# Kernel optimization log

Measured on AMD Instinct MI355X. Metric: run time of the kernel, lower is better.

Reference implementation:

```python
import jax, jax.numpy as jnp
import numpy as np

B, T, PHYS = 256, 64, 3        # batch of initial conditions, time steps, physical dim
LAT, NN, NHID = 8, 128, 3      # latent dim, hidden width, num hidden layers
WIN, PRED = 32, 64             # Hankel window, num_pred_steps


def _mlp(x, w_in, b_in, w_h, b_h, w_out, b_out):
    # Dense stack: relu hidden layers, linear output (ae_output_activation='linear')
    h = jax.nn.relu(x @ w_in + b_in)
    for i in range(w_h.shape[0]):
        h = jax.nn.relu(h @ w_h[i] + b_h[i])
    return h @ w_out + b_out


def _hankel_dmd(y):
    # y: [B, L, T] latent trajectories (already transposed as in call())
    Bsz, L, Tn = y.shape
    R = Tn - (WIN - 1)                                   # num_rows_hankel
    # Vectorized Hankel build (replaces nested TensorArray loops):
    idx = jnp.arange(R)[:, None] + jnp.arange(WIN)[None, :]
    H = y[:, :, idx].reshape(Bsz, L * R, WIN)
    Ym, Yp = H[:, :, :-1], H[:, :, 1:]
    # Exact DMD operator A = Yp V Sig^-1 U^H (full M x M, as in the TF code)
    U, sig, Vh = jnp.linalg.svd(Ym, full_matrices=False)
    V = jnp.swapaxes(Vh, -1, -2)
    A = Yp @ (V / sig[:, None, :]) @ jnp.swapaxes(U, -1, -2)     # [B, M, M]
    A = jax.lax.stop_gradient(A)   # no-op in fwd; eig has no JAX grad rule
    evals, evecs = jnp.linalg.eig(A)                             # complex64: [B,M], [B,M,M]
    Phi = jnp.linalg.solve(evecs, Ym.astype(evecs.dtype))
    y0 = Phi[:, :, 0]                                            # [B, M]
    evecs_s = evecs[:, ::R, :]                                   # stride = R -> [B, L, M]
    # Vectorized replacement of the sequential recon loop: evals^k for k=0..P-1
    powers = evals[:, None, :] ** jnp.arange(PRED)[None, :, None]  # [B, P, M]
    modes = powers * y0[:, None, :]                                # [B, P, M]
    recon = jnp.real(jnp.einsum('blm,bpm->bpl', evecs_s, modes))   # [B, P, L]
    return recon


def setup_inputs() -> dict:
    ks = jax.random.split(jax.random.key(0), 8)

    def w(k, fi, fo):
        return jax.random.normal(k, (fi, fo), jnp.float32) / np.sqrt(fi)

    def wh(k, f):
        return jax.random.normal(k, (NHID, f, f), jnp.float32) / np.sqrt(f)

    return {
        'x': jax.random.normal(ks[0], (B, T, PHYS), jnp.float32),
        'enc_w_in': w(ks[1], PHYS, NN), 'enc_b_in': jnp.zeros((NN,), jnp.float32),
        'enc_w_h': wh(ks[2], NN), 'enc_b_h': jnp.zeros((NHID, NN), jnp.float32),
        'enc_w_out': w(ks[3], NN, LAT), 'enc_b_out': jnp.zeros((LAT,), jnp.float32),
        'dec_w_in': w(ks[4], LAT, NN), 'dec_b_in': jnp.zeros((NN,), jnp.float32),
        'dec_w_h': wh(ks[5], NN), 'dec_b_h': jnp.zeros((NHID, NN), jnp.float32),
        'dec_w_out': w(ks[6], NN, PHYS), 'dec_b_out': jnp.zeros((PHYS,), jnp.float32),
    }


def reference(x, enc_w_in, enc_b_in, enc_w_h, enc_b_h, enc_w_out, enc_b_out,
              dec_w_in, dec_b_in, dec_w_h, dec_b_h, dec_w_out, dec_b_out):
    y = _mlp(x, enc_w_in, enc_b_in, enc_w_h, enc_b_h, enc_w_out, enc_b_out)        # [B, T, LAT]
    x_ae = _mlp(y, dec_w_in, dec_b_in, dec_w_h, dec_b_h, dec_w_out, dec_b_out)     # [B, T, PHYS]
    y_adv = _hankel_dmd(jnp.swapaxes(y, 1, 2))                                     # [B, PRED, LAT]
    x_adv = _mlp(y_adv, dec_w_in, dec_b_in, dec_w_h, dec_b_h, dec_w_out, dec_b_out)  # [B, PRED, PHYS]
    return (y, x_ae, x_adv, y_adv)
```

## Files before the change

kernel.cpp:

```cpp
#include <hip/hip_runtime.h>
#include <math.h>

namespace {
constexpr int kB = 256;
constexpr int kT = 64;
constexpr int kPhys = 3;
constexpr int kLat = 8;
constexpr int kNN = 128;
constexpr int kWin = 32;
constexpr int kPred = 64;
constexpr int kHRow = 132;
constexpr int kThreads = 1024;
constexpr int kWUnit = 8 * 4 * 64 * 8;
constexpr int kUS = 50688;
}

typedef short bf16x8 __attribute__((ext_vector_type(8)));
typedef float f32x4 __attribute__((ext_vector_type(4)));

__device__ __forceinline__ double rdlane_f64(double x, int l) {
  const long long v = __double_as_longlong(x);
  const int lo = __builtin_amdgcn_readlane((int)(unsigned int)(v & 0xffffffffll), l);
  const int hi = __builtin_amdgcn_readlane((int)(v >> 32), l);
  const long long r = (((long long)hi) << 32) | (unsigned long long)(unsigned int)lo;
  return __longlong_as_double(r);
}

__device__ __forceinline__ unsigned rneb(float f) {
  const unsigned u = __float_as_uint(f);
  return (u + 0x7fffu + ((u >> 16) & 1u)) >> 16;
}
__device__ __forceinline__ void split3(float a, short& s1, short& s2, short& s3) {
  const unsigned b1 = rneb(a);
  const float f1 = __uint_as_float(b1 << 16);
  const float r1 = a - f1;
  const unsigned b2 = rneb(r1);
  const float f2 = __uint_as_float(b2 << 16);
  s1 = (short)b1; s2 = (short)b2; s3 = (short)rneb(r1 - f2);
}
__device__ __forceinline__ void split2(float a, short& s1, short& s2) {
  const unsigned b1 = rneb(a);
  const float f1 = __uint_as_float(b1 << 16);
  s1 = (short)b1; s2 = (short)rneb(a - f1);
}

__global__ __launch_bounds__(256) void split_weights_kernel(
    const float* __restrict__ ewh, const float* __restrict__ dwh,
    short* __restrict__ wfrag)
{
  const int gid = blockIdx.x * 256 + threadIdx.x;
  const int l = gid & 63;
  const int q = (gid >> 6) & 3;
  const int n = (gid >> 8) & 7;
  const int layer = gid >> 11;
  const bool enc = layer < 3;
  const float* __restrict__ W = enc ? (ewh + (size_t)layer * kNN * kNN)
                                    : (dwh + (size_t)(layer - 3) * kNN * kNN);
  const int colg = 16 * n + (l & 15);
  const int krow = 8 * (l >> 4);
  bf16x8 p1, p2, p3;
#pragma unroll
  for (int e = 0; e < 8; ++e) {
    const float wv = W[(32 * q + krow + e) * kNN + colg];
    short s1, s2, s3; split3(wv, s1, s2, s3);
    p1[e] = s1; p2[e] = s2; p3[e] = s3;
  }
  const int off = ((n * 4 + q) * 64 + l) * 8;
  if (enc) {
    const size_t base = (size_t)(layer * 3) * kWUnit;
    *(bf16x8*)&wfrag[base + off] = p1;
    *(bf16x8*)&wfrag[base + kWUnit + off] = p2;
    *(bf16x8*)&wfrag[base + 2 * kWUnit + off] = p3;
  } else {
    const size_t base = (size_t)(9 + (layer - 3) * 2) * kWUnit;
    *(bf16x8*)&wfrag[base + off] = p1;
    *(bf16x8*)&wfrag[base + kWUnit + off] = p2;
  }
}

template<int MPW, int SPLITS, bool TO_FRAG>
__device__ __forceinline__ void mfma_scatter(
    const short* __restrict__ Bfrag, const float* __restrict__ bias,
    const short* __restrict__ fragIn, void* __restrict__ out, int tid)
{
  constexpr int MT = 2 * MPW;
  constexpr int PLANE = MT * 4 * 64 * 8;
  const int w = tid >> 6, l = tid & 63;
  const int n = w & 7, m0 = (w >> 3) * MPW;
  const int colg = 16 * n + (l & 15);
  bf16x8 B1[4], B2[4], B3[4];
#pragma unroll
  for (int q = 0; q < 4; ++q) {
    const int boff = ((n * 4 + q) * 64 + l) * 8;
    B1[q] = *(const bf16x8*)&Bfrag[boff];
    B2[q] = *(const bf16x8*)&Bfrag[kWUnit + boff];
    if constexpr (SPLITS == 3) B3[q] = *(const bf16x8*)&Bfrag[2 * kWUnit + boff];
  }
  const float bj = bias[colg];
  f32x4 acc[MPW];
#pragma unroll
  for (int mi = 0; mi < MPW; ++mi) acc[mi] = {bj, bj, bj, bj};
#pragma unroll
  for (int q = 0; q < 4; ++q) {
#pragma unroll
    for (int mi = 0; mi < MPW; ++mi) {
      const int o = (((m0 + mi) * 4 + q) * 64 + l) * 8;
      const bf16x8 a1 = *(const bf16x8*)&fragIn[o];
      const bf16x8 a2 = *(const bf16x8*)&fragIn[PLANE + o];
      acc[mi] = __builtin_amdgcn_mfma_f32_16x16x32_bf16(a1, B1[q], acc[mi], 0, 0, 0);
      acc[mi] = __builtin_amdgcn_mfma_f32_16x16x32_bf16(a1, B2[q], acc[mi], 0, 0, 0);
      acc[mi] = __builtin_amdgcn_mfma_f32_16x16x32_bf16(a2, B1[q], acc[mi], 0, 0, 0);
      if constexpr (SPLITS == 3) {
        const bf16x8 a3 = *(const bf16x8*)&fragIn[2 * PLANE + o];
        acc[mi] = __builtin_amdgcn_mfma_f32_16x16x32_bf16(a1, B3[q], acc[mi], 0, 0, 0);
        acc[mi] = __builtin_amdgcn_mfma_f32_16x16x32_bf16(a2, B2[q], acc[mi], 0, 0, 0);
        acc[mi] = __builtin_amdgcn_mfma_f32_16x16x32_bf16(a3, B1[q], acc[mi], 0, 0, 0);
      }
    }
  }
  const int rbase = (l >> 4) * 4;
  if constexpr (TO_FRAG) {
    short* __restrict__ f = (short*)out;
    const int qt = colg >> 5, sub = (colg >> 3) & 3, et = colg & 7;
#pragma unroll
    for (int mi = 0; mi < MPW; ++mi)
#pragma unroll
      for (int r = 0; r < 4; ++r) {
        const float v = fmaxf(acc[mi][r], 0.f);
        const int off = (((m0 + mi) * 4 + qt) * 64 + (rbase + r + 16 * sub)) * 8 + et;
        if constexpr (SPLITS == 3) {
          short s1, s2, s3; split3(v, s1, s2, s3);
          f[off] = s1; f[PLANE + off] = s2; f[2 * PLANE + off] = s3;
        } else {
          short s1, s2; split2(v, s1, s2);
          f[off] = s1; f[PLANE + off] = s2;
        }
      }
  } else {
    float* __restrict__ hb = (float*)out;
#pragma unroll
    for (int mi = 0; mi < MPW; ++mi)
#pragma unroll
      for (int r = 0; r < 4; ++r)
        hb[(16 * (m0 + mi) + rbase + r) * kHRow + colg] = fmaxf(acc[mi][r], 0.f);
  }
}

__global__ __launch_bounds__(kThreads, 4) void fused_kernel(
    const float* __restrict__ x,
    const float* __restrict__ ewin, const float* __restrict__ ebin,
    const float* __restrict__ ebh,
    const float* __restrict__ ewout,const float* __restrict__ ebout,
    const float* __restrict__ dwin, const float* __restrict__ dbin,
    const float* __restrict__ dbh,
    const float* __restrict__ dwout,const float* __restrict__ dbout,
    const short* __restrict__ wfrag,
    float* __restrict__ y_g, float* __restrict__ xae_g,
    float* __restrict__ xadv_g, float* __restrict__ yadv_g)
{
  __shared__ __align__(16) char US1[kUS];
  __shared__ __align__(16) char US2[kUS];
  __shared__ float ybuf[kT * kLat];
  __shared__ float yadv2[kWin * kLat];

  const int tid = threadIdx.x;
  const int b = blockIdx.x;

  double* dmd  = (double*)US1;
  double* yd   = dmd;
  double* P    = dmd + 520;
  double* Corr = dmd + 2664;
  double* KTm  = dmd + 3720;
  double* Dv   = dmd + 4743;

  constexpr int PE = 4 * 4 * 64 * 8;
  constexpr int PD = 6 * 4 * 64 * 8;

  {
    short* __restrict__ f = (short*)US1;
    const float* __restrict__ xg = x + (size_t)b * kT * kPhys;
    const int j = tid & 127, rg = tid >> 7;
    const float w0 = ewin[j], w1 = ewin[kNN + j], w2 = ewin[2 * kNN + j];
    const float bj = ebin[j];
    const int qt = j >> 5, sub = (j >> 3) & 3, et = j & 7;
#pragma unroll
    for (int rr = 0; rr < 8; ++rr) {
      const int r = rg * 8 + rr;
      const float* __restrict__ xr = xg + r * 3;
      const float a = fmaxf(bj + xr[0] * w0 + xr[1] * w1 + xr[2] * w2, 0.f);
      short s1, s2, s3; split3(a, s1, s2, s3);
      const int off = (((r >> 4) * 4 + qt) * 64 + ((r & 15) + 16 * sub)) * 8 + et;
      f[off] = s1; f[PE + off] = s2; f[2 * PE + off] = s3;
    }
  }
  __syncthreads();

  mfma_scatter<2, 3, true >(wfrag + (size_t)0 * kWUnit, ebh + 0 * kNN, (short*)US1, US2, tid);
  __syncthreads();
  mfma_scatter<2, 3, true >(wfrag + (size_t)3 * kWUnit, ebh + 1 * kNN, (short*)US2, US1, tid);
  __syncthreads();
  mfma_scatter<2, 3, false>(wfrag + (size_t)6 * kWUnit, ebh + 2 * kNN, (short*)US1, US2, tid);
  __syncthreads();

  if (tid < 512) {
    const float* __restrict__ hb = (const float*)US2;
    const int r = tid >> 3, o = tid & 7;
    float a = ebout[o];
    for (int k4 = 0; k4 < kNN; k4 += 4) {
      const float4 hv = *(const float4*)&hb[r * kHRow + k4];
      a += hv.x * ewout[(k4 + 0) * kLat + o] + hv.y * ewout[(k4 + 1) * kLat + o]
         + hv.z * ewout[(k4 + 2) * kLat + o] + hv.w * ewout[(k4 + 3) * kLat + o];
    }
    ybuf[r * kLat + o] = a;
    y_g[(size_t)b * kT * kLat + tid] = a;
    yd[o * 65 + r] = (double)a;
  }
  __syncthreads();

  {
    for (int idx = tid; idx < 32 * 64; idx += kThreads) {
      const int d = idx >> 6, t = idx & 63;
      if (t + d < kT) {
        double s = 0.0;
#pragma unroll
        for (int l = 0; l < kLat; ++l) s += yd[l * 65 + t] * yd[l * 65 + t + d];
        P[d * 67 + t] = s;
      }
    }
    __syncthreads();

    {
      const int a = tid >> 5, c = tid & 31;
      const int d = (c >= a) ? (c - a) : (a - c);
      const int base = (c >= a) ? a : c;
      double s0 = 0.0, s1 = 0.0;
#pragma unroll
      for (int r = 0; r < 32; r += 2) { s0 += P[d * 67 + base + r]; s1 += P[d * 67 + base + r + 1]; }
      Corr[a * 33 + c] = s0 + s1 + P[d * 67 + base + 32];
    }
    __syncthreads();

    if (tid < 64) {
      const int lane = tid;
      const int colidx = (lane <= 30) ? lane : (lane <= 61 ? lane - 30 : 1);
      double m[31];
#pragma unroll
      for (int i = 0; i < 31; ++i) m[i] = Corr[i * 33 + colidx];
#pragma unroll
      for (int k = 0; k < 31; ++k) {
        const double piv = rdlane_f64(m[k], k);
        const double pinv = 1.0 / piv;
        m[k] *= pinv;
#pragma unroll
        for (int i = 0; i < 31; ++i) {
          if (i == k) continue;
          const double bci = rdlane_f64(m[i], k);
          m[i] = fma(-bci, m[k], m[i]);
        }
      }
      if (lane >= 31 && lane < 62) {
        const int c = lane - 31;
#pragma unroll
        for (int i = 0; i < 31; ++i) KTm[i * 33 + c] = m[i];
      }
      const int ri = (lane < 31) ? lane : 0;
      double Kr[31];
#pragma unroll
      for (int j = 0; j < 31; ++j) Kr[j] = KTm[ri * 33 + j];

      double dv = Kr[30];
      if (lane < 31) Dv[0 * 33 + lane] = dv;
      for (int k = 0; k < 31; ++k) {
        double a0 = 0.0, a1 = 0.0, a2 = 0.0, a3 = 0.0;
#pragma unroll
        for (int j = 0; j < 31; ++j) {
          const double dj = rdlane_f64(dv, j);
          if ((j & 3) == 0) a0 = fma(Kr[j], dj, a0);
          else if ((j & 3) == 1) a1 = fma(Kr[j], dj, a1);
          else if ((j & 3) == 2) a2 = fma(Kr[j], dj, a2);
          else a3 = fma(Kr[j], dj, a3);
        }
        dv = (a0 + a1) + (a2 + a3);
        if (lane < 31) Dv[(k + 1) * 33 + lane] = dv;
      }
    }
    __syncthreads();

    float* __restrict__ ob = yadv_g + (size_t)b * kPred * kLat;
    if (tid < 256) {
      ob[tid] = ybuf[tid];
    } else if (tid < 512) {
      const int q = tid - 256;
      const int k = q >> 3, l = q & 7;
      double a0 = 0.0, a1 = 0.0, a2 = 0.0, a3 = 0.0;
#pragma unroll
      for (int j = 0; j < 31; ++j) {
        const double t = yd[l * 65 + j + 1];
        if ((j & 3) == 0) a0 = fma(t, Dv[k * 33 + j], a0);
        else if ((j & 3) == 1) a1 = fma(t, Dv[k * 33 + j], a1);
        else if ((j & 3) == 2) a2 = fma(t, Dv[k * 33 + j], a2);
        else a3 = fma(t, Dv[k * 33 + j], a3);
      }
      const float v = (float)((a0 + a1) + (a2 + a3));
      ob[256 + q] = v;
      yadv2[q] = v;
    }
    __syncthreads();
  }

  {
    short* __restrict__ f = (short*)US2;
    const int j = tid & 127, rg = tid >> 7;
    float wr[kLat];
#pragma unroll
    for (int k = 0; k < kLat; ++k) wr[k] = dwin[k * kNN + j];
    const float bj = dbin[j];
    const int qt = j >> 5, sub = (j >> 3) & 3, et = j & 7;
#pragma unroll
    for (int rr = 0; rr < 12; ++rr) {
      const int r = rg * 12 + rr;
      const float* __restrict__ src = (r < kT) ? &ybuf[r * kLat] : &yadv2[(r - kT) * kLat];
      float a = bj;
#pragma unroll
      for (int k = 0; k < kLat; ++k) a += src[k] * wr[k];
      a = fmaxf(a, 0.f);
      short s1, s2; split2(a, s1, s2);
      const int off = (((r >> 4) * 4 + qt) * 64 + ((r & 15) + 16 * sub)) * 8 + et;
      f[off] = s1; f[PD + off] = s2;
    }
  }
  __syncthreads();

  mfma_scatter<3, 2, true >(wfrag + (size_t)9  * kWUnit, dbh + 0 * kNN, (short*)US2, US1, tid);
  __syncthreads();
  mfma_scatter<3, 2, true >(wfrag + (size_t)11 * kWUnit, dbh + 1 * kNN, (short*)US1, US2, tid);
  __syncthreads();
  mfma_scatter<3, 2, false>(wfrag + (size_t)13 * kWUnit, dbh + 2 * kNN, (short*)US2, US1, tid);
  __syncthreads();

  if (tid < 96 * kPhys) {
    const float* __restrict__ hb = (const float*)US1;
    const int r = tid / 3, o = tid - r * 3;
    float a = dbout[o];
    for (int k4 = 0; k4 < kNN; k4 += 4) {
      const float4 hv = *(const float4*)&hb[r * kHRow + k4];
      a += hv.x * dwout[(k4 + 0) * kPhys + o] + hv.y * dwout[(k4 + 1) * kPhys + o]
         + hv.z * dwout[(k4 + 2) * kPhys + o] + hv.w * dwout[(k4 + 3) * kPhys + o];
    }
    if (r < kT) {
      xae_g[(size_t)b * kT * kPhys + tid] = a;
      if (r < kWin) xadv_g[(size_t)b * kT * kPhys + tid] = a;
    } else {
      const int rr = r - kT + kWin;
      xadv_g[(size_t)b * kT * kPhys + rr * kPhys + o] = a;
    }
  }
}

extern "C" void kernel_launch(void* const* d_in, const int* in_sizes, int n_in,
                              void* d_out, int out_size, void* d_ws, size_t ws_size,
                              hipStream_t stream)
{
  const float* x         = (const float*)d_in[0];
  const float* enc_w_in  = (const float*)d_in[1];
  const float* enc_b_in  = (const float*)d_in[2];
  const float* enc_w_h   = (const float*)d_in[3];
  const float* enc_b_h   = (const float*)d_in[4];
  const float* enc_w_out = (const float*)d_in[5];
  const float* enc_b_out = (const float*)d_in[6];
  const float* dec_w_in  = (const float*)d_in[7];
  const float* dec_b_in  = (const float*)d_in[8];
  const float* dec_w_h   = (const float*)d_in[9];
  const float* dec_b_h   = (const float*)d_in[10];
  const float* dec_w_out = (const float*)d_in[11];
  const float* dec_b_out = (const float*)d_in[12];

  float* out   = (float*)d_out;
  float* y     = out;
  float* x_ae  = out + (size_t)kB * kT * kLat;
  float* x_adv = x_ae + (size_t)kB * kT * kPhys;
  float* y_adv = x_adv + (size_t)kB * kT * kPhys;

  short* wfrag = (short*)d_ws;

  split_weights_kernel<<<48, 256, 0, stream>>>(enc_w_h, dec_w_h, wfrag);
  fused_kernel<<<kB, kThreads, 0, stream>>>(
      x, enc_w_in, enc_b_in, enc_b_h, enc_w_out, enc_b_out,
      dec_w_in, dec_b_in, dec_b_h, dec_w_out, dec_b_out,
      wfrag, y, x_ae, x_adv, y_adv);
}
```

Measured before the change: 55.89 us.

## Split fused kernel into encoder, DMD, and decoder kernels with row-split blocks

```diff
diff --git a/kernel.cpp b/kernel.cpp
--- a/kernel.cpp
+++ b/kernel.cpp
@@ -10,9 +10,7 @@
 constexpr int kWin = 32;
 constexpr int kPred = 64;
 constexpr int kHRow = 132;
-constexpr int kThreads = 1024;
 constexpr int kWUnit = 8 * 4 * 64 * 8;
-constexpr int kUS = 50688;
 }
 
 typedef short bf16x8 __attribute__((ext_vector_type(8)));
@@ -78,15 +76,13 @@
   }
 }
 
-template<int MPW, int SPLITS, bool TO_FRAG>
-__device__ __forceinline__ void mfma_scatter(
+template<int MT, int SPLITS, bool TO_FRAG>
+__device__ __forceinline__ void mfma_layer8(
     const short* __restrict__ Bfrag, const float* __restrict__ bias,
     const short* __restrict__ fragIn, void* __restrict__ out, int tid)
 {
-  constexpr int MT = 2 * MPW;
   constexpr int PLANE = MT * 4 * 64 * 8;
-  const int w = tid >> 6, l = tid & 63;
-  const int n = w & 7, m0 = (w >> 3) * MPW;
+  const int n = (tid >> 6) & 7, l = tid & 63;
   const int colg = 16 * n + (l & 15);
   bf16x8 B1[4], B2[4], B3[4];
 #pragma unroll
@@ -97,14 +93,14 @@
     if constexpr (SPLITS == 3) B3[q] = *(const bf16x8*)&Bfrag[2 * kWUnit + boff];
   }
   const float bj = bias[colg];
-  f32x4 acc[MPW];
-#pragma unroll
-  for (int mi = 0; mi < MPW; ++mi) acc[mi] = {bj, bj, bj, bj};
+  f32x4 acc[MT];
+#pragma unroll
+  for (int mi = 0; mi < MT; ++mi) acc[mi] = {bj, bj, bj, bj};
 #pragma unroll
   for (int q = 0; q < 4; ++q) {
 #pragma unroll
-    for (int mi = 0; mi < MPW; ++mi) {
-      const int o = (((m0 + mi) * 4 + q) * 64 + l) * 8;
+    for (int mi = 0; mi < MT; ++mi) {
+      const int o = ((mi * 4 + q) * 64 + l) * 8;
       const bf16x8 a1 = *(const bf16x8*)&fragIn[o];
       const bf16x8 a2 = *(const bf16x8*)&fragIn[PLANE + o];
       acc[mi] = __builtin_amdgcn_mfma_f32_16x16x32_bf16(a1, B1[q], acc[mi], 0, 0, 0);
@@ -123,11 +119,11 @@
     short* __restrict__ f = (short*)out;
     const int qt = colg >> 5, sub = (colg >> 3) & 3, et = colg & 7;
 #pragma unroll
-    for (int mi = 0; mi < MPW; ++mi)
+    for (int mi = 0; mi < MT; ++mi)
 #pragma unroll
       for (int r = 0; r < 4; ++r) {
         const float v = fmaxf(acc[mi][r], 0.f);
-        const int off = (((m0 + mi) * 4 + qt) * 64 + (rbase + r + 16 * sub)) * 8 + et;
+        const int off = ((mi * 4 + qt) * 64 + (rbase + r + 16 * sub)) * 8 + et;
         if constexpr (SPLITS == 3) {
           short s1, s2, s3; split3(v, s1, s2, s3);
           f[off] = s1; f[PLANE + off] = s2; f[2 * PLANE + off] = s3;
@@ -139,46 +135,29 @@
   } else {
     float* __restrict__ hb = (float*)out;
 #pragma unroll
-    for (int mi = 0; mi < MPW; ++mi)
+    for (int mi = 0; mi < MT; ++mi)
 #pragma unroll
       for (int r = 0; r < 4; ++r)
-        hb[(16 * (m0 + mi) + rbase + r) * kHRow + colg] = fmaxf(acc[mi][r], 0.f);
-  }
-}
-
-__global__ __launch_bounds__(kThreads, 4) void fused_kernel(
+        hb[(16 * mi + rbase + r) * kHRow + colg] = fmaxf(acc[mi][r], 0.f);
+  }
+}
+
+__global__ __launch_bounds__(512, 4) void enc_kernel(
     const float* __restrict__ x,
     const float* __restrict__ ewin, const float* __restrict__ ebin,
     const float* __restrict__ ebh,
     const float* __restrict__ ewout,const float* __restrict__ ebout,
-    const float* __restrict__ dwin, const float* __restrict__ dbin,
-    const float* __restrict__ dbh,
-    const float* __restrict__ dwout,const float* __restrict__ dbout,
-    const short* __restrict__ wfrag,
-    float* __restrict__ y_g, float* __restrict__ xae_g,
-    float* __restrict__ xadv_g, float* __restrict__ yadv_g)
-{
-  __shared__ __align__(16) char US1[kUS];
-  __shared__ __align__(16) char US2[kUS];
-  __shared__ float ybuf[kT * kLat];
-  __shared__ float yadv2[kWin * kLat];
-
+    const short* __restrict__ wfrag, float* __restrict__ y_g)
+{
+  constexpr int PE = 2 * 4 * 64 * 8;
+  __shared__ __align__(16) char US1[24576];
+  __shared__ __align__(16) char US2[24576];
   const int tid = threadIdx.x;
-  const int b = blockIdx.x;
-
-  double* dmd  = (double*)US1;
-  double* yd   = dmd;
-  double* P    = dmd + 520;
-  double* Corr = dmd + 2664;
-  double* KTm  = dmd + 3720;
-  double* Dv   = dmd + 4743;
-
-  constexpr int PE = 4 * 4 * 64 * 8;
-  constexpr int PD = 6 * 4 * 64 * 8;
+  const int b = blockIdx.x >> 1;
+  const int r0 = (blockIdx.x & 1) * 32;
 
   {
     short* __restrict__ f = (short*)US1;
-    const float* __restrict__ xg = x + (size_t)b * kT * kPhys;
     const int j = tid & 127, rg = tid >> 7;
     const float w0 = ewin[j], w1 = ewin[kNN + j], w2 = ewin[2 * kNN + j];
     const float bj = ebin[j];
@@ -186,7 +165,7 @@
 #pragma unroll
     for (int rr = 0; rr < 8; ++rr) {
       const int r = rg * 8 + rr;
-      const float* __restrict__ xr = xg + r * 3;
+      const float* __restrict__ xr = x + ((size_t)b * kT + r0 + r) * kPhys;
       const float a = fmaxf(bj + xr[0] * w0 + xr[1] * w1 + xr[2] * w2, 0.f);
       short s1, s2, s3; split3(a, s1, s2, s3);
       const int off = (((r >> 4) * 4 + qt) * 64 + ((r & 15) + 16 * sub)) * 8 + et;
@@ -194,15 +173,14 @@
     }
   }
   __syncthreads();
-
-  mfma_scatter<2, 3, true >(wfrag + (size_t)0 * kWUnit, ebh + 0 * kNN, (short*)US1, US2, tid);
-  __syncthreads();
-  mfma_scatter<2, 3, true >(wfrag + (size_t)3 * kWUnit, ebh + 1 * kNN, (short*)US2, US1, tid);
-  __syncthreads();
-  mfma_scatter<2, 3, false>(wfrag + (size_t)6 * kWUnit, ebh + 2 * kNN, (short*)US1, US2, tid);
-  __syncthreads();
-
-  if (tid < 512) {
+  mfma_layer8<2, 3, true >(wfrag + (size_t)0 * kWUnit, ebh + 0 * kNN, (short*)US1, US2, tid);
+  __syncthreads();
+  mfma_layer8<2, 3, true >(wfrag + (size_t)3 * kWUnit, ebh + 1 * kNN, (short*)US2, US1, tid);
+  __syncthreads();
+  mfma_layer8<2, 3, false>(wfrag + (size_t)6 * kWUnit, ebh + 2 * kNN, (short*)US1, US2, tid);
+  __syncthreads();
+
+  if (tid < 256) {
     const float* __restrict__ hb = (const float*)US2;
     const int r = tid >> 3, o = tid & 7;
     float a = ebout[o];
@@ -211,105 +189,143 @@
       a += hv.x * ewout[(k4 + 0) * kLat + o] + hv.y * ewout[(k4 + 1) * kLat + o]
          + hv.z * ewout[(k4 + 2) * kLat + o] + hv.w * ewout[(k4 + 3) * kLat + o];
     }
-    ybuf[r * kLat + o] = a;
-    y_g[(size_t)b * kT * kLat + tid] = a;
-    yd[o * 65 + r] = (double)a;
-  }
-  __syncthreads();
+    y_g[(size_t)b * kT * kLat + (r0 + r) * kLat + o] = a;
+  }
+}
+
+__global__ __launch_bounds__(512) void dmd_kernel(const float* __restrict__ y_g,
+                                                  float* __restrict__ yadv_g)
+{
+  __shared__ __align__(16) char US[46400];
+  double* dmd  = (double*)US;
+  double* yd   = dmd;
+  double* P    = dmd + 520;
+  double* Corr = dmd + 2664;
+  double* KTm  = dmd + 3720;
+  double* Dv   = dmd + 4743;
+  const int tid = threadIdx.x;
+  const int b = blockIdx.x;
+  const float* __restrict__ yb = y_g + (size_t)b * kT * kLat;
 
   {
-    for (int idx = tid; idx < 32 * 64; idx += kThreads) {
-      const int d = idx >> 6, t = idx & 63;
-      if (t + d < kT) {
-        double s = 0.0;
-#pragma unroll
-        for (int l = 0; l < kLat; ++l) s += yd[l * 65 + t] * yd[l * 65 + t + d];
-        P[d * 67 + t] = s;
+    const int r = tid >> 3, o = tid & 7;
+    yd[o * 65 + r] = (double)yb[tid];
+  }
+  __syncthreads();
+
+  for (int idx = tid; idx < 32 * 64; idx += 512) {
+    const int d = idx >> 6, t = idx & 63;
+    if (t + d < kT) {
+      double s = 0.0;
+#pragma unroll
+      for (int l = 0; l < kLat; ++l) s += yd[l * 65 + t] * yd[l * 65 + t + d];
+      P[d * 67 + t] = s;
+    }
+  }
+  __syncthreads();
+
+  for (int idx = tid; idx < 32 * 32; idx += 512) {
+    const int a = idx >> 5, c = idx & 31;
+    const int d = (c >= a) ? (c - a) : (a - c);
+    const int base = (c >= a) ? a : c;
+    double s0 = 0.0, s1 = 0.0;
+#pragma unroll
+    for (int r = 0; r < 32; r += 2) { s0 += P[d * 67 + base + r]; s1 += P[d * 67 + base + r + 1]; }
+    Corr[a * 33 + c] = s0 + s1 + P[d * 67 + base + 32];
+  }
+  __syncthreads();
+
+  if (tid < 64) {
+    const int lane = tid;
+    const int colidx = (lane <= 30) ? lane : (lane <= 61 ? lane - 30 : 1);
+    double m[31];
+#pragma unroll
+    for (int i = 0; i < 31; ++i) m[i] = Corr[i * 33 + colidx];
+#pragma unroll
+    for (int k = 0; k < 31; ++k) {
+      const double piv = rdlane_f64(m[k], k);
+      const double pinv = 1.0 / piv;
+      m[k] *= pinv;
+#pragma unroll
+      for (int i = 0; i < 31; ++i) {
+        if (i == k) continue;
+        const double bci = rdlane_f64(m[i], k);
+        m[i] = fma(-bci, m[k], m[i]);
       }
     }
-    __syncthreads();
-
-    {
-      const int a = tid >> 5, c = tid & 31;
-      const int d = (c >= a) ? (c - a) : (a - c);
-      const int base = (c >= a) ? a : c;
-      double s0 = 0.0, s1 = 0.0;
-#pragma unroll
-      for (int r = 0; r < 32; r += 2) { s0 += P[d * 67 + base + r]; s1 += P[d * 67 + base + r + 1]; }
-      Corr[a * 33 + c] = s0 + s1 + P[d * 67 + base + 32];
-    }
-    __syncthreads();
-
-    if (tid < 64) {
-      const int lane = tid;
-      const int colidx = (lane <= 30) ? lane : (lane <= 61 ? lane - 30 : 1);
-      double m[31];
-#pragma unroll
-      for (int i = 0; i < 31; ++i) m[i] = Corr[i * 33 + colidx];
-#pragma unroll
-      for (int k = 0; k < 31; ++k) {
-        const double piv = rdlane_f64(m[k], k);
-        const double pinv = 1.0 / piv;
-        m[k] *= pinv;
-#pragma unroll
-        for (int i = 0; i < 31; ++i) {
-          if (i == k) continue;
-          const double bci = rdlane_f64(m[i], k);
-          m[i] = fma(-bci, m[k], m[i]);
-        }
+    if (lane >= 31 && lane < 62) {
+      const int c = lane - 31;
+#pragma unroll
+      for (int i = 0; i < 31; ++i) KTm[i * 33 + c] = m[i];
+    }
+    const int ri = (lane < 31) ? lane : 0;
+    double Kr[31];
+#pragma unroll
+    for (int j = 0; j < 31; ++j) Kr[j] = KTm[ri * 33 + j];
+
+    double dv = Kr[30];
+    if (lane < 31) Dv[0 * 33 + lane] = dv;
+    for (int k = 0; k < 31; ++k) {
+      double a0 = 0.0, a1 = 0.0, a2 = 0.0, a3 = 0.0;
+#pragma unroll
+      for (int j = 0; j < 31; ++j) {
+        const double dj = rdlane_f64(dv, j);
+        if ((j & 3) == 0) a0 = fma(Kr[j], dj, a0);
+        else if ((j & 3) == 1) a1 = fma(Kr[j], dj, a1);
+        else if ((j & 3) == 2) a2 = fma(Kr[j], dj, a2);
+        else a3 = fma(Kr[j], dj, a3);
       }
-      if (lane >= 31 && lane < 62) {
-        const int c = lane - 31;
-#pragma unroll
-        for (int i = 0; i < 31; ++i) KTm[i * 33 + c] = m[i];
-      }
-      const int ri = (lane < 31) ? lane : 0;
-      double Kr[31];
-#pragma unroll
-      for (int j = 0; j < 31; ++j) Kr[j] = KTm[ri * 33 + j];
-
-      double dv = Kr[30];
-      if (lane < 31) Dv[0 * 33 + lane] = dv;
-      for (int k = 0; k < 31; ++k) {
-        double a0 = 0.0, a1 = 0.0, a2 = 0.0, a3 = 0.0;
-#pragma unroll
-        for (int j = 0; j < 31; ++j) {
-          const double dj = rdlane_f64(dv, j);
-          if ((j & 3) == 0) a0 = fma(Kr[j], dj, a0);
-          else if ((j & 3) == 1) a1 = fma(Kr[j], dj, a1);
-          else if ((j & 3) == 2) a2 = fma(Kr[j], dj, a2);
-          else a3 = fma(Kr[j], dj, a3);
-        }
-        dv = (a0 + a1) + (a2 + a3);
-        if (lane < 31) Dv[(k + 1) * 33 + lane] = dv;
-      }
-    }
-    __syncthreads();
-
-    float* __restrict__ ob = yadv_g + (size_t)b * kPred * kLat;
-    if (tid < 256) {
-      ob[tid] = ybuf[tid];
-    } else if (tid < 512) {
-      const int q = tid - 256;
-      const int k = q >> 3, l = q & 7;
-      double a0 = 0.0, a1 = 0.0, a2 = 0.0, a3 = 0.0;
-#pragma unroll
-      for (int j = 0; j < 31; ++j) {
-        const double t = yd[l * 65 + j + 1];
-        if ((j & 3) == 0) a0 = fma(t, Dv[k * 33 + j], a0);
-        else if ((j & 3) == 1) a1 = fma(t, Dv[k * 33 + j], a1);
-        else if ((j & 3) == 2) a2 = fma(t, Dv[k * 33 + j], a2);
-        else a3 = fma(t, Dv[k * 33 + j], a3);
-      }
-      const float v = (float)((a0 + a1) + (a2 + a3));
-      ob[256 + q] = v;
-      yadv2[q] = v;
-    }
-    __syncthreads();
-  }
+      dv = (a0 + a1) + (a2 + a3);
+      if (lane < 31) Dv[(k + 1) * 33 + lane] = dv;
+    }
+  }
+  __syncthreads();
+
+  float* __restrict__ ob = yadv_g + (size_t)b * kPred * kLat;
+  if (tid < 256) {
+    ob[tid] = yb[tid];
+  } else {
+    const int q = tid - 256;
+    const int k = q >> 3, l = q & 7;
+    double a0 = 0.0, a1 = 0.0, a2 = 0.0, a3 = 0.0;
+#pragma unroll
+    for (int j = 0; j < 31; ++j) {
+      const double t = yd[l * 65 + j + 1];
+      if ((j & 3) == 0) a0 = fma(t, Dv[k * 33 + j], a0);
+      else if ((j & 3) == 1) a1 = fma(t, Dv[k * 33 + j], a1);
+      else if ((j & 3) == 2) a2 = fma(t, Dv[k * 33 + j], a2);
+      else a3 = fma(t, Dv[k * 33 + j], a3);
+    }
+    ob[256 + q] = (float)((a0 + a1) + (a2 + a3));
+  }
+}
+
+__global__ __launch_bounds__(512, 4) void dec_kernel(
+    const float* __restrict__ y_g, const float* __restrict__ yadv_g,
+    const float* __restrict__ dwin, const float* __restrict__ dbin,
+    const float* __restrict__ dbh,
+    const float* __restrict__ dwout,const float* __restrict__ dbout,
+    const short* __restrict__ wfrag,
+    float* __restrict__ xae_g, float* __restrict__ xadv_g)
+{
+  constexpr int PD = 3 * 4 * 64 * 8;
+  __shared__ __align__(16) char US1[25344];
+  __shared__ __align__(16) char US2[25344];
+  __shared__ float src48[48 * kLat];
+  const int tid = threadIdx.x;
+  const int b = blockIdx.x >> 1;
+  const int R0 = (blockIdx.x & 1) * 48;
+
+  for (int i = tid; i < 48 * kLat; i += 512) {
+    const int r = i >> 3, o = i & 7;
+    const int gr = R0 + r;
+    src48[i] = (gr < kT) ? y_g[(size_t)b * kT * kLat + gr * kLat + o]
+                         : yadv_g[(size_t)b * kPred * kLat + (gr - kWin) * kLat + o];
+  }
+  __syncthreads();
 
   {
-    short* __restrict__ f = (short*)US2;
+    short* __restrict__ f = (short*)US1;
     const int j = tid & 127, rg = tid >> 7;
     float wr[kLat];
 #pragma unroll
@@ -319,7 +335,7 @@
 #pragma unroll
     for (int rr = 0; rr < 12; ++rr) {
       const int r = rg * 12 + rr;
-      const float* __restrict__ src = (r < kT) ? &ybuf[r * kLat] : &yadv2[(r - kT) * kLat];
+      const float* __restrict__ src = &src48[r * kLat];
       float a = bj;
 #pragma unroll
       for (int k = 0; k < kLat; ++k) a += src[k] * wr[k];
@@ -330,28 +346,28 @@
     }
   }
   __syncthreads();
-
-  mfma_scatter<3, 2, true >(wfrag + (size_t)9  * kWUnit, dbh + 0 * kNN, (short*)US2, US1, tid);
-  __syncthreads();
-  mfma_scatter<3, 2, true >(wfrag + (size_t)11 * kWUnit, dbh + 1 * kNN, (short*)US1, US2, tid);
-  __syncthreads();
-  mfma_scatter<3, 2, false>(wfrag + (size_t)13 * kWUnit, dbh + 2 * kNN, (short*)US2, US1, tid);
-  __syncthreads();
-
-  if (tid < 96 * kPhys) {
-    const float* __restrict__ hb = (const float*)US1;
+  mfma_layer8<3, 2, true >(wfrag + (size_t)9  * kWUnit, dbh + 0 * kNN, (short*)US1, US2, tid);
+  __syncthreads();
+  mfma_layer8<3, 2, true >(wfrag + (size_t)11 * kWUnit, dbh + 1 * kNN, (short*)US2, US1, tid);
+  __syncthreads();
+  mfma_layer8<3, 2, false>(wfrag + (size_t)13 * kWUnit, dbh + 2 * kNN, (short*)US1, US2, tid);
+  __syncthreads();
+
+  if (tid < 48 * kPhys) {
+    const float* __restrict__ hb = (const float*)US2;
     const int r = tid / 3, o = tid - r * 3;
+    const int gr = R0 + r;
     float a = dbout[o];
     for (int k4 = 0; k4 < kNN; k4 += 4) {
       const float4 hv = *(const float4*)&hb[r * kHRow + k4];
       a += hv.x * dwout[(k4 + 0) * kPhys + o] + hv.y * dwout[(k4 + 1) * kPhys + o]
          + hv.z * dwout[(k4 + 2) * kPhys + o] + hv.w * dwout[(k4 + 3) * kPhys + o];
     }
-    if (r < kT) {
-      xae_g[(size_t)b * kT * kPhys + tid] = a;
-      if (r < kWin) xadv_g[(size_t)b * kT * kPhys + tid] = a;
+    if (gr < kT) {
+      xae_g[(size_t)b * kT * kPhys + gr * kPhys + o] = a;
+      if (gr < kWin) xadv_g[(size_t)b * kT * kPhys + gr * kPhys + o] = a;
     } else {
-      const int rr = r - kT + kWin;
+      const int rr = gr - kT + kWin;
       xadv_g[(size_t)b * kT * kPhys + rr * kPhys + o] = a;
     }
   }
@@ -384,8 +400,10 @@
   short* wfrag = (short*)d_ws;
 
   split_weights_kernel<<<48, 256, 0, stream>>>(enc_w_h, dec_w_h, wfrag);
-  fused_kernel<<<kB, kThreads, 0, stream>>>(
-      x, enc_w_in, enc_b_in, enc_b_h, enc_w_out, enc_b_out,
-      dec_w_in, dec_b_in, dec_b_h, dec_w_out, dec_b_out,
-      wfrag, y, x_ae, x_adv, y_adv);
-}
+  enc_kernel<<<2 * kB, 512, 0, stream>>>(
+      x, enc_w_in, enc_b_in, enc_b_h, enc_w_out, enc_b_out, wfrag, y);
+  dmd_kernel<<<kB, 512, 0, stream>>>(y, y_adv);
+  dec_kernel<<<2 * kB, 512, 0, stream>>>(
+      y, y_adv, dec_w_in, dec_b_in, dec_b_h, dec_w_out, dec_b_out,
+      wfrag, x_ae, x_adv);
+}
```

Measured after the change: 57.29 us. +2.5%, slower.

## Overlap serial DMD solve with decoder MLP on autoencoder rows

Applied to the files above, without the earlier changes.

```diff
diff --git a/kernel.cpp b/kernel.cpp
--- a/kernel.cpp
+++ b/kernel.cpp
@@ -12,7 +12,6 @@
 constexpr int kHRow = 132;
 constexpr int kThreads = 1024;
 constexpr int kWUnit = 8 * 4 * 64 * 8;
-constexpr int kUS = 50688;
 }
 
 typedef short bf16x8 __attribute__((ext_vector_type(8)));
@@ -79,7 +78,7 @@
 }
 
 template<int MPW, int SPLITS, bool TO_FRAG>
-__device__ __forceinline__ void mfma_scatter(
+__device__ __forceinline__ void mfma_enc(
     const short* __restrict__ Bfrag, const float* __restrict__ bias,
     const short* __restrict__ fragIn, void* __restrict__ out, int tid)
 {
@@ -128,13 +127,8 @@
       for (int r = 0; r < 4; ++r) {
         const float v = fmaxf(acc[mi][r], 0.f);
         const int off = (((m0 + mi) * 4 + qt) * 64 + (rbase + r + 16 * sub)) * 8 + et;
-        if constexpr (SPLITS == 3) {
-          short s1, s2, s3; split3(v, s1, s2, s3);
-          f[off] = s1; f[PLANE + off] = s2; f[2 * PLANE + off] = s3;
-        } else {
-          short s1, s2; split2(v, s1, s2);
-          f[off] = s1; f[PLANE + off] = s2;
-        }
+        short s1, s2, s3; split3(v, s1, s2, s3);
+        f[off] = s1; f[PLANE + off] = s2; f[2 * PLANE + off] = s3;
       }
   } else {
     float* __restrict__ hb = (float*)out;
@@ -143,6 +137,59 @@
 #pragma unroll
       for (int r = 0; r < 4; ++r)
         hb[(16 * (m0 + mi) + rbase + r) * kHRow + colg] = fmaxf(acc[mi][r], 0.f);
+  }
+}
+
+template<int MTN, bool TO_FRAG>
+__device__ __forceinline__ void mfma_dec(
+    const short* __restrict__ Bfrag, const float* __restrict__ bias,
+    const short* __restrict__ fragIn, void* __restrict__ out, int n, int l)
+{
+  constexpr int PLANE = MTN * 4 * 64 * 8;
+  const int colg = 16 * n + (l & 15);
+  bf16x8 B1[4], B2[4];
+#pragma unroll
+  for (int q = 0; q < 4; ++q) {
+    const int boff = ((n * 4 + q) * 64 + l) * 8;
+    B1[q] = *(const bf16x8*)&Bfrag[boff];
+    B2[q] = *(const bf16x8*)&Bfrag[kWUnit + boff];
+  }
+  const float bj = bias[colg];
+  f32x4 acc[MTN];
+#pragma unroll
+  for (int mi = 0; mi < MTN; ++mi) acc[mi] = {bj, bj, bj, bj};
+#pragma unroll
+  for (int q = 0; q < 4; ++q) {
+#pragma unroll
+    for (int mi = 0; mi < MTN; ++mi) {
+      const int o = ((mi * 4 + q) * 64 + l) * 8;
+      const bf16x8 a1 = *(const bf16x8*)&fragIn[o];
+      const bf16x8 a2 = *(const bf16x8*)&fragIn[PLANE + o];
+      acc[mi] = __builtin_amdgcn_mfma_f32_16x16x32_bf16(a1, B1[q], acc[mi], 0, 0, 0);
+      acc[mi] = __builtin_amdgcn_mfma_f32_16x16x32_bf16(a1, B2[q], acc[mi], 0, 0, 0);
+      acc[mi] = __builtin_amdgcn_mfma_f32_16x16x32_bf16(a2, B1[q], acc[mi], 0, 0, 0);
+    }
+  }
+  const int rbase = (l >> 4) * 4;
+  if constexpr (TO_FRAG) {
+    short* __restrict__ f = (short*)out;
+    const int qt = colg >> 5, sub = (colg >> 3) & 3, et = colg & 7;
+#pragma unroll
+    for (int mi = 0; mi < MTN; ++mi)
+#pragma unroll
+      for (int r = 0; r < 4; ++r) {
+        const float v = fmaxf(acc[mi][r], 0.f);
+        const int off = ((mi * 4 + qt) * 64 + (rbase + r + 16 * sub)) * 8 + et;
+        short s1, s2; split2(v, s1, s2);
+        f[off] = s1; f[PLANE + off] = s2;
+      }
+  } else {
+    float* __restrict__ hb = (float*)out;
+#pragma unroll
+    for (int mi = 0; mi < MTN; ++mi)
+#pragma unroll
+      for (int r = 0; r < 4; ++r)
+        hb[(16 * mi + rbase + r) * kHRow + colg] = fmaxf(acc[mi][r], 0.f);
   }
 }
 
@@ -158,26 +205,32 @@
     float* __restrict__ y_g, float* __restrict__ xae_g,
     float* __restrict__ xadv_g, float* __restrict__ yadv_g)
 {
-  __shared__ __align__(16) char US1[kUS];
-  __shared__ __align__(16) char US2[kUS];
-  __shared__ float ybuf[kT * kLat];
-  __shared__ float yadv2[kWin * kLat];
+  __shared__ __align__(16) char bufA[50688];
+  __shared__ __align__(16) char bufB[50688];
+  __shared__ __align__(16) double dmdS[5280];
+  __shared__ float ybuf[512];
+  __shared__ float yadv2[256];
+  __shared__ float xstash[192];
+
+  double* P    = dmdS;
+  double* Corr = dmdS + 2144;
+  double* KTm  = dmdS + 3200;
+  double* Dv   = dmdS + 4223;
+
+  short* fragA_G1 = (short*)bufA;
+  short* fragA_G2 = (short*)(bufA + 32768);
+  short* fragB_G1 = (short*)bufB;
+  short* fragB_G2 = (short*)(bufB + 33792);
+  float* hbB_G1   = (float*)bufB;
+  float* hbA_G2   = (float*)bufA;
 
   const int tid = threadIdx.x;
+  const int l64 = tid & 63;
   const int b = blockIdx.x;
 
-  double* dmd  = (double*)US1;
-  double* yd   = dmd;
-  double* P    = dmd + 520;
-  double* Corr = dmd + 2664;
-  double* KTm  = dmd + 3720;
-  double* Dv   = dmd + 4743;
-
-  constexpr int PE = 4 * 4 * 64 * 8;
-  constexpr int PD = 6 * 4 * 64 * 8;
-
   {
-    short* __restrict__ f = (short*)US1;
+    constexpr int PE = 4 * 4 * 64 * 8;
+    short* __restrict__ f = (short*)bufA;
     const float* __restrict__ xg = x + (size_t)b * kT * kPhys;
     const int j = tid & 127, rg = tid >> 7;
     const float w0 = ewin[j], w1 = ewin[kNN + j], w2 = ewin[2 * kNN + j];
@@ -195,15 +248,15 @@
   }
   __syncthreads();
 
-  mfma_scatter<2, 3, true >(wfrag + (size_t)0 * kWUnit, ebh + 0 * kNN, (short*)US1, US2, tid);
-  __syncthreads();
-  mfma_scatter<2, 3, true >(wfrag + (size_t)3 * kWUnit, ebh + 1 * kNN, (short*)US2, US1, tid);
-  __syncthreads();
-  mfma_scatter<2, 3, false>(wfrag + (size_t)6 * kWUnit, ebh + 2 * kNN, (short*)US1, US2, tid);
+  mfma_enc<2, 3, true >(wfrag + (size_t)0 * kWUnit, ebh + 0 * kNN, (short*)bufA, bufB, tid);
+  __syncthreads();
+  mfma_enc<2, 3, true >(wfrag + (size_t)3 * kWUnit, ebh + 1 * kNN, (short*)bufB, bufA, tid);
+  __syncthreads();
+  mfma_enc<2, 3, false>(wfrag + (size_t)6 * kWUnit, ebh + 2 * kNN, (short*)bufA, bufB, tid);
   __syncthreads();
 
   if (tid < 512) {
-    const float* __restrict__ hb = (const float*)US2;
+    const float* __restrict__ hb = (const float*)bufB;
     const int r = tid >> 3, o = tid & 7;
     float a = ebout[o];
     for (int k4 = 0; k4 < kNN; k4 += 4) {
@@ -211,115 +264,34 @@
       a += hv.x * ewout[(k4 + 0) * kLat + o] + hv.y * ewout[(k4 + 1) * kLat + o]
          + hv.z * ewout[(k4 + 2) * kLat + o] + hv.w * ewout[(k4 + 3) * kLat + o];
     }
-    ybuf[r * kLat + o] = a;
-    y_g[(size_t)b * kT * kLat + tid] = a;
-    yd[o * 65 + r] = (double)a;
-  }
-  __syncthreads();
-
-  {
-    for (int idx = tid; idx < 32 * 64; idx += kThreads) {
+    ybuf[tid] = a;
+  }
+  __syncthreads();
+
+  if (tid < 512) {
+    for (int idx = tid; idx < 32 * 64; idx += 512) {
       const int d = idx >> 6, t = idx & 63;
       if (t + d < kT) {
         double s = 0.0;
 #pragma unroll
-        for (int l = 0; l < kLat; ++l) s += yd[l * 65 + t] * yd[l * 65 + t + d];
+        for (int l = 0; l < kLat; ++l)
+          s += (double)ybuf[t * 8 + l] * (double)ybuf[(t + d) * 8 + l];
         P[d * 67 + t] = s;
       }
     }
-    __syncthreads();
-
-    {
-      const int a = tid >> 5, c = tid & 31;
-      const int d = (c >= a) ? (c - a) : (a - c);
-      const int base = (c >= a) ? a : c;
-      double s0 = 0.0, s1 = 0.0;
-#pragma unroll
-      for (int r = 0; r < 32; r += 2) { s0 += P[d * 67 + base + r]; s1 += P[d * 67 + base + r + 1]; }
-      Corr[a * 33 + c] = s0 + s1 + P[d * 67 + base + 32];
-    }
-    __syncthreads();
-
-    if (tid < 64) {
-      const int lane = tid;
-      const int colidx = (lane <= 30) ? lane : (lane <= 61 ? lane - 30 : 1);
-      double m[31];
-#pragma unroll
-      for (int i = 0; i < 31; ++i) m[i] = Corr[i * 33 + colidx];
-#pragma unroll
-      for (int k = 0; k < 31; ++k) {
-        const double piv = rdlane_f64(m[k], k);
-        const double pinv = 1.0 / piv;
-        m[k] *= pinv;
-#pragma unroll
-        for (int i = 0; i < 31; ++i) {
-          if (i == k) continue;
-          const double bci = rdlane_f64(m[i], k);
-          m[i] = fma(-bci, m[k], m[i]);
-        }
-      }
-      if (lane >= 31 && lane < 62) {
-        const int c = lane - 31;
-#pragma unroll
-        for (int i = 0; i < 31; ++i) KTm[i * 33 + c] = m[i];
-      }
-      const int ri = (lane < 31) ? lane : 0;
-      double Kr[31];
-#pragma unroll
-      for (int j = 0; j < 31; ++j) Kr[j] = KTm[ri * 33 + j];
-
-      double dv = Kr[30];
-      if (lane < 31) Dv[0 * 33 + lane] = dv;
-      for (int k = 0; k < 31; ++k) {
-        double a0 = 0.0, a1 = 0.0, a2 = 0.0, a3 = 0.0;
-#pragma unroll
-        for (int j = 0; j < 31; ++j) {
-          const double dj = rdlane_f64(dv, j);
-          if ((j & 3) == 0) a0 = fma(Kr[j], dj, a0);
-          else if ((j & 3) == 1) a1 = fma(Kr[j], dj, a1);
-          else if ((j & 3) == 2) a2 = fma(Kr[j], dj, a2);
-          else a3 = fma(Kr[j], dj, a3);
-        }
-        dv = (a0 + a1) + (a2 + a3);
-        if (lane < 31) Dv[(k + 1) * 33 + lane] = dv;
-      }
-    }
-    __syncthreads();
-
-    float* __restrict__ ob = yadv_g + (size_t)b * kPred * kLat;
-    if (tid < 256) {
-      ob[tid] = ybuf[tid];
-    } else if (tid < 512) {
-      const int q = tid - 256;
-      const int k = q >> 3, l = q & 7;
-      double a0 = 0.0, a1 = 0.0, a2 = 0.0, a3 = 0.0;
-#pragma unroll
-      for (int j = 0; j < 31; ++j) {
-        const double t = yd[l * 65 + j + 1];
-        if ((j & 3) == 0) a0 = fma(t, Dv[k * 33 + j], a0);
-        else if ((j & 3) == 1) a1 = fma(t, Dv[k * 33 + j], a1);
-        else if ((j & 3) == 2) a2 = fma(t, Dv[k * 33 + j], a2);
-        else a3 = fma(t, Dv[k * 33 + j], a3);
-      }
-      const float v = (float)((a0 + a1) + (a2 + a3));
-      ob[256 + q] = v;
-      yadv2[q] = v;
-    }
-    __syncthreads();
-  }
-
-  {
-    short* __restrict__ f = (short*)US2;
-    const int j = tid & 127, rg = tid >> 7;
+  } else {
+    constexpr int PD = 4 * 4 * 64 * 8;
+    short* __restrict__ f = fragA_G1;
+    const int j = tid & 127, rg = (tid >> 7) - 4;
     float wr[kLat];
 #pragma unroll
     for (int k = 0; k < kLat; ++k) wr[k] = dwin[k * kNN + j];
     const float bj = dbin[j];
     const int qt = j >> 5, sub = (j >> 3) & 3, et = j & 7;
 #pragma unroll
-    for (int rr = 0; rr < 12; ++rr) {
-      const int r = rg * 12 + rr;
-      const float* __restrict__ src = (r < kT) ? &ybuf[r * kLat] : &yadv2[(r - kT) * kLat];
+    for (int rr = 0; rr < 16; ++rr) {
+      const int r = rg * 16 + rr;
+      const float* __restrict__ src = &ybuf[r * kLat];
       float a = bj;
 #pragma unroll
       for (int k = 0; k < kLat; ++k) a += src[k] * wr[k];
@@ -331,28 +303,160 @@
   }
   __syncthreads();
 
-  mfma_scatter<3, 2, true >(wfrag + (size_t)9  * kWUnit, dbh + 0 * kNN, (short*)US2, US1, tid);
-  __syncthreads();
-  mfma_scatter<3, 2, true >(wfrag + (size_t)11 * kWUnit, dbh + 1 * kNN, (short*)US1, US2, tid);
-  __syncthreads();
-  mfma_scatter<3, 2, false>(wfrag + (size_t)13 * kWUnit, dbh + 2 * kNN, (short*)US2, US1, tid);
-  __syncthreads();
-
-  if (tid < 96 * kPhys) {
-    const float* __restrict__ hb = (const float*)US1;
+  {
+    const int a = tid >> 5, c = tid & 31;
+    const int d = (c >= a) ? (c - a) : (a - c);
+    const int base = (c >= a) ? a : c;
+    double s0 = 0.0, s1 = 0.0;
+#pragma unroll
+    for (int r = 0; r < 32; r += 2) { s0 += P[d * 67 + base + r]; s1 += P[d * 67 + base + r + 1]; }
+    Corr[a * 33 + c] = s0 + s1 + P[d * 67 + base + 32];
+  }
+  __syncthreads();
+
+  if (tid < 64) {
+    const int lane = tid;
+    const int colidx = (lane <= 30) ? lane : (lane <= 61 ? lane - 30 : 1);
+    double m[31];
+#pragma unroll
+    for (int i = 0; i < 31; ++i) m[i] = Corr[i * 33 + colidx];
+#pragma unroll
+    for (int k = 0; k < 31; ++k) {
+      const double piv = rdlane_f64(m[k], k);
+      const double pinv = 1.0 / piv;
+      m[k] *= pinv;
+#pragma unroll
+      for (int i = 0; i < 31; ++i) {
+        if (i == k) continue;
+        const double bci = rdlane_f64(m[i], k);
+        m[i] = fma(-bci, m[k], m[i]);
+      }
+    }
+    if (lane >= 31 && lane < 62) {
+      const int c = lane - 31;
+#pragma unroll
+      for (int i = 0; i < 31; ++i) KTm[i * 33 + c] = m[i];
+    }
+    const int ri = (lane < 31) ? lane : 0;
+    double Kr[31];
+#pragma unroll
+    for (int j = 0; j < 31; ++j) Kr[j] = KTm[ri * 33 + j];
+    double dv = Kr[30];
+    if (lane < 31) Dv[0 * 33 + lane] = dv;
+    for (int k = 0; k < 31; ++k) {
+      double a0 = 0.0, a1 = 0.0, a2 = 0.0, a3 = 0.0;
+#pragma unroll
+      for (int j = 0; j < 31; ++j) {
+        const double dj = rdlane_f64(dv, j);
+        if ((j & 3) == 0) a0 = fma(Kr[j], dj, a0);
+        else if ((j & 3) == 1) a1 = fma(Kr[j], dj, a1);
+        else if ((j & 3) == 2) a2 = fma(Kr[j], dj, a2);
+        else a3 = fma(Kr[j], dj, a3);
+      }
+      dv = (a0 + a1) + (a2 + a3);
+      if (lane < 31) Dv[(k + 1) * 33 + lane] = dv;
+    }
+  } else if (tid >= 512) {
+    mfma_dec<4, true>(wfrag + (size_t)9 * kWUnit, dbh + 0 * kNN,
+                      fragA_G1, fragB_G1, (tid >> 6) - 8, l64);
+  }
+  __syncthreads();
+
+  if (tid < 512) {
+    mfma_dec<4, true>(wfrag + (size_t)11 * kWUnit, dbh + 1 * kNN,
+                      fragB_G1, fragA_G1, tid >> 6, l64);
+  } else if (tid < 768) {
+    const int q = tid - 512;
+    const int k = q >> 3, l = q & 7;
+    double a0 = 0.0, a1 = 0.0, a2 = 0.0, a3 = 0.0;
+#pragma unroll
+    for (int j = 0; j < 31; ++j) {
+      const double t = (double)ybuf[(j + 1) * 8 + l];
+      if ((j & 3) == 0) a0 = fma(t, Dv[k * 33 + j], a0);
+      else if ((j & 3) == 1) a1 = fma(t, Dv[k * 33 + j], a1);
+      else if ((j & 3) == 2) a2 = fma(t, Dv[k * 33 + j], a2);
+      else a3 = fma(t, Dv[k * 33 + j], a3);
+    }
+    yadv2[q] = (float)((a0 + a1) + (a2 + a3));
+  }
+  __syncthreads();
+
+  if (tid < 512) {
+    mfma_dec<4, false>(wfrag + (size_t)13 * kWUnit, dbh + 2 * kNN,
+                       fragA_G1, hbB_G1, tid >> 6, l64);
+  } else {
+    constexpr int PD = 2 * 4 * 64 * 8;
+    short* __restrict__ f = fragA_G2;
+    const int j = tid & 127, rg = (tid >> 7) - 4;
+    float wr[kLat];
+#pragma unroll
+    for (int k = 0; k < kLat; ++k) wr[k] = dwin[k * kNN + j];
+    const float bj = dbin[j];
+    const int qt = j >> 5, sub = (j >> 3) & 3, et = j & 7;
+#pragma unroll
+    for (int rr = 0; rr < 8; ++rr) {
+      const int r = 64 + rg * 8 + rr;
+      const float* __restrict__ src = &yadv2[(r - kT) * kLat];
+      float a = bj;
+#pragma unroll
+      for (int k = 0; k < kLat; ++k) a += src[k] * wr[k];
+      a = fmaxf(a, 0.f);
+      short s1, s2; split2(a, s1, s2);
+      const int mi = (r - 64) >> 4;
+      const int off = ((mi * 4 + qt) * 64 + ((r & 15) + 16 * sub)) * 8 + et;
+      f[off] = s1; f[PD + off] = s2;
+    }
+  }
+  __syncthreads();
+
+  if (tid < 192) {
     const int r = tid / 3, o = tid - r * 3;
     float a = dbout[o];
     for (int k4 = 0; k4 < kNN; k4 += 4) {
-      const float4 hv = *(const float4*)&hb[r * kHRow + k4];
+      const float4 hv = *(const float4*)&hbB_G1[r * kHRow + k4];
       a += hv.x * dwout[(k4 + 0) * kPhys + o] + hv.y * dwout[(k4 + 1) * kPhys + o]
          + hv.z * dwout[(k4 + 2) * kPhys + o] + hv.w * dwout[(k4 + 3) * kPhys + o];
     }
-    if (r < kT) {
-      xae_g[(size_t)b * kT * kPhys + tid] = a;
-      if (r < kWin) xadv_g[(size_t)b * kT * kPhys + tid] = a;
-    } else {
-      const int rr = r - kT + kWin;
-      xadv_g[(size_t)b * kT * kPhys + rr * kPhys + o] = a;
+    xstash[tid] = a;
+  } else if (tid >= 512) {
+    mfma_dec<2, true>(wfrag + (size_t)9 * kWUnit, dbh + 0 * kNN,
+                      fragA_G2, fragB_G2, (tid >> 6) - 8, l64);
+  }
+  __syncthreads();
+
+  if (tid >= 512) {
+    mfma_dec<2, true>(wfrag + (size_t)11 * kWUnit, dbh + 1 * kNN,
+                      fragB_G2, fragA_G2, (tid >> 6) - 8, l64);
+  }
+  __syncthreads();
+
+  if (tid < 512) {
+    mfma_dec<2, false>(wfrag + (size_t)13 * kWUnit, dbh + 2 * kNN,
+                       fragA_G2, hbA_G2, tid >> 6, l64);
+  }
+  __syncthreads();
+
+  if (tid < 96) {
+    const int r = tid / 3, o = tid - r * 3;
+    float a = dbout[o];
+    for (int k4 = 0; k4 < kNN; k4 += 4) {
+      const float4 hv = *(const float4*)&hbA_G2[r * kHRow + k4];
+      a += hv.x * dwout[(k4 + 0) * kPhys + o] + hv.y * dwout[(k4 + 1) * kPhys + o]
+         + hv.z * dwout[(k4 + 2) * kPhys + o] + hv.w * dwout[(k4 + 3) * kPhys + o];
+    }
+    xadv_g[(size_t)b * kT * kPhys + (r + 32) * kPhys + o] = a;
+  } else {
+    for (int i = tid - 96; i < 192 + 512 + 512; i += kThreads - 96) {
+      if (i < 192) {
+        xae_g[(size_t)b * kT * kPhys + i] = xstash[i];
+        if (i < 96) xadv_g[(size_t)b * kT * kPhys + i] = xstash[i];
+      } else if (i < 704) {
+        const int q = i - 192;
+        yadv_g[(size_t)b * kPred * kLat + q] = (q < 256) ? ybuf[q] : yadv2[q - 256];
+      } else {
+        const int q = i - 704;
+        y_g[(size_t)b * kT * kLat + q] = ybuf[q];
+      }
     }
   }
 }
```

Result: no change. 55.38 us (-0.9%).
